# Kernel optimization log

Measured on AMD Instinct MI355X. Metric: run time of the kernel, lower is better.

The kernel has to match this reference:

```python
import jax, jax.numpy as jnp
import numpy as np

B, T, F = 16, 512, 512
H, D = 8, 64  # heads, key_dim (latent_dim)
EPS = 1e-3    # keras LayerNormalization default epsilon


def layer_norm(x, g, b):
    mu = jnp.mean(x, axis=-1, keepdims=True)
    var = jnp.mean(jnp.square(x - mu), axis=-1, keepdims=True)
    return (x - mu) * jax.lax.rsqrt(var + EPS) * g + b


def setup_inputs() -> dict:
    key = jax.random.key(0)
    ks = jax.random.split(key, 16)
    s = 0.02
    return {
        "x": jax.random.normal(ks[0], (B, T, F), jnp.float32),
        # MultiHeadAttention params (keras layout)
        "Wq": jax.random.normal(ks[1], (F, H, D), jnp.float32) * s,
        "bq": jnp.zeros((H, D), jnp.float32),
        "Wk": jax.random.normal(ks[2], (F, H, D), jnp.float32) * s,
        "bk": jnp.zeros((H, D), jnp.float32),
        "Wv": jax.random.normal(ks[3], (F, H, D), jnp.float32) * s,
        "bv": jnp.zeros((H, D), jnp.float32),
        "Wo": jax.random.normal(ks[4], (H, D, F), jnp.float32) * s,
        "bo": jnp.zeros((F,), jnp.float32),
        "ln1_g": jnp.ones((F,), jnp.float32),
        "ln1_b": jnp.zeros((F,), jnp.float32),
        # GRU (reset_after=True, recurrent_activation=sigmoid, activation=relu)
        "gru_k": jax.random.normal(ks[5], (F, 3 * F), jnp.float32) * s,
        "gru_rk": jax.random.normal(ks[6], (F, 3 * F), jnp.float32) * s,
        "gru_b": jnp.zeros((2, 3 * F), jnp.float32),  # [input_bias, recurrent_bias]
        # Dense
        "Wd": jax.random.normal(ks[7], (F, F), jnp.float32) * s,
        "bd": jnp.zeros((F,), jnp.float32),
        "ln2_g": jnp.ones((F,), jnp.float32),
        "ln2_b": jnp.zeros((F,), jnp.float32),
    }


def mha(x, Wq, bq, Wk, bk, Wv, bv, Wo, bo):
    q = jnp.einsum("btf,fhd->bthd", x, Wq) + bq
    k = jnp.einsum("bsf,fhd->bshd", x, Wk) + bk
    v = jnp.einsum("bsf,fhd->bshd", x, Wv) + bv
    scores = jnp.einsum("bthd,bshd->bhts", q, k) / jnp.sqrt(jnp.float32(D))
    attn = jax.nn.softmax(scores, axis=-1)
    ctx = jnp.einsum("bhts,bshd->bthd", attn, v)
    return jnp.einsum("bthd,hdf->btf", ctx, Wo) + bo


def gru(x, gru_k, gru_rk, gru_b):
    # keras GRU, reset_after=True: precompute input projections once
    xp = x @ gru_k + gru_b[0]            # [B,T,3F]
    rb = gru_b[1]                        # recurrent bias [3F]
    xp_t = jnp.transpose(xp, (1, 0, 2))  # time-major [T,B,3F]

    def step(h, xt):
        rec = h @ gru_rk + rb
        xz, xr, xh = jnp.split(xt, 3, axis=-1)
        rz, rr, rh = jnp.split(rec, 3, axis=-1)
        z = jax.nn.sigmoid(xz + rz)
        r = jax.nn.sigmoid(xr + rr)
        hh = jax.nn.relu(xh + r * rh)    # activation='relu'
        h_new = z * h + (1.0 - z) * hh
        return h_new, h_new

    h0 = jnp.zeros((x.shape[0], gru_rk.shape[0]), x.dtype)
    _, ys = jax.lax.scan(step, h0, xp_t)
    return jnp.transpose(ys, (1, 0, 2))  # [B,T,F]


def reference(x, Wq, bq, Wk, bk, Wv, bv, Wo, bo, ln1_g, ln1_b,
              gru_k, gru_rk, gru_b, Wd, bd, ln2_g, ln2_b):
    a = mha(x, Wq, bq, Wk, bk, Wv, bv, Wo, bo)
    x1 = layer_norm(a + x, ln1_g, ln1_b)
    g = gru(x1, gru_k, gru_rk, gru_b)
    d = g @ Wd + bd
    return layer_norm(d + x1, ln2_g, ln2_b)
```

## Files before the change

### kernel.cpp

```cpp
#include <hip/hip_runtime.h>
#include <math.h>

#define GRID_WGS 128

typedef __attribute__((ext_vector_type(8))) short bf16x8;
typedef __attribute__((ext_vector_type(4))) float f32x4;
typedef __attribute__((ext_vector_type(4))) unsigned short us4;

static __device__ __forceinline__ float sigmoidf_(float x) {
    return 1.0f / (1.0f + __expf(-x));
}
static __device__ __forceinline__ unsigned short f2bf(float f) {
    unsigned int u = __float_as_uint(f);
    u += 0x7fffu + ((u >> 16) & 1u);
    return (unsigned short)(u >> 16);
}
static __device__ __forceinline__ float bfbits2f(unsigned int b) {
    return __uint_as_float(b << 16);
}
static __device__ __forceinline__ void gload_lds16(const void* g, void* l) {
    __builtin_amdgcn_global_load_lds(
        (const __attribute__((address_space(1))) unsigned int*)g,
        (__attribute__((address_space(3))) unsigned int*)l, 16, 0, 0);
}

__global__ __launch_bounds__(256)
void prep(const float* __restrict__ x, unsigned short* __restrict__ xb,
          const float* __restrict__ bq, const float* __restrict__ bk,
          const float* __restrict__ bv, float* __restrict__ bqkv,
          const float* __restrict__ Wq, const float* __restrict__ Wk,
          const float* __restrict__ Wv, const float* __restrict__ Wo,
          const float* __restrict__ gruk, const float* __restrict__ Wd,
          unsigned short* __restrict__ wqkvT, unsigned short* __restrict__ woT,
          unsigned short* __restrict__ gkT, unsigned short* __restrict__ wdT,
          unsigned int* __restrict__ hbufz, unsigned int* __restrict__ Z)
{
    __shared__ float tile[32][33];
    const int bid = blockIdx.x, tid = threadIdx.x;
    if (bid < 4096) {
        const int i = (bid * 256 + tid) * 4;
        const float4 v = *(const float4*)(x + i);
        const us4 o = {f2bf(v.x), f2bf(v.y), f2bf(v.z), f2bf(v.w)};
        *(us4*)(xb + i) = o;
    } else if (bid < 4102) {
        const int i = (bid - 4096) * 256 + tid;
        bqkv[i] = (i < 512) ? bq[i] : ((i < 1024) ? bk[i - 512] : bv[i - 1024]);
    } else if (bid < 6150) {
        int t = bid - 4102;
        const float* in; unsigned short* out; int N;
        if      (t < 256)  { in = Wq;   out = wqkvT;               N = 512;  }
        else if (t < 512)  { in = Wk;   out = wqkvT + 256 * 1024;  N = 512;  t -= 256;  }
        else if (t < 768)  { in = Wv;   out = wqkvT + 512 * 1024;  N = 512;  t -= 512;  }
        else if (t < 1024) { in = Wo;   out = woT;                 N = 512;  t -= 768;  }
        else if (t < 1792) { in = gruk; out = gkT;                 N = 1536; t -= 1024; }
        else               { in = Wd;   out = wdT;                 N = 512;  t -= 1792; }
        const int tilesx = N / 32;
        const int n0 = (t % tilesx) * 32, k0 = (t / tilesx) * 32;
        const int c = tid & 31, r8 = tid >> 5;
#pragma unroll
        for (int i = 0; i < 4; ++i) {
            const int k = r8 + i * 8;
            tile[k][c] = in[(size_t)(k0 + k) * N + n0 + c];
        }
        __syncthreads();
#pragma unroll
        for (int i = 0; i < 4; ++i) {
            const int n = r8 + i * 8;
            out[(size_t)(n0 + n) * 512 + k0 + c] = f2bf(tile[c][n]);
        }
    } else if (bid == 6150) {
        for (int i = tid; i < 8192; i += 256) hbufz[i] = 0u;
    } else {
        for (int i = tid; i < 2048; i += 256) Z[i] = 0u;
    }
}

__global__ __launch_bounds__(256)
void gemm_bf16(const unsigned short* __restrict__ A, const unsigned short* __restrict__ Bt,
               const float* __restrict__ bias, const float* __restrict__ resid,
               float* __restrict__ C, unsigned short* __restrict__ Cb,
               int M, int N, int K)
{
    __shared__ unsigned short As[128 * 64];
    __shared__ unsigned short Bs[128 * 64];
    const int tid = threadIdx.x;
    const int wave = tid >> 6, lane = tid & 63;
    const int bm = blockIdx.x * 128, bn = blockIdx.y * 128;
    const int wr = wave >> 1, wc = wave & 1;
    const int stR = lane >> 3;
    const int stC = (lane & 7) * 8;

    const unsigned short* Abase = A + (size_t)(bm + wave * 32 + stR) * K + stC;
    const unsigned short* Bbase = Bt + (size_t)(bn + wave * 32 + stR) * K + stC;
    unsigned short* AsW = As + wave * 2048;
    unsigned short* BsW = Bs + wave * 2048;

    f32x4 acc[4][4] = {};
    const int fr = lane & 15;
    const int fko = (lane >> 4) * 8;

    for (int k0 = 0; k0 < K; k0 += 64) {
#pragma unroll
        for (int i = 0; i < 4; ++i) {
            gload_lds16(Abase + (size_t)i * 8 * K + k0, AsW + i * 512);
            gload_lds16(Bbase + (size_t)i * 8 * K + k0, BsW + i * 512);
        }
        __syncthreads();
        bf16x8 af[4][2], bfr[4][2];
#pragma unroll
        for (int m = 0; m < 4; ++m) {
            const unsigned short* ap = As + (wr * 64 + m * 16 + fr) * 64 + fko;
            af[m][0] = *(const bf16x8*)(ap);
            af[m][1] = *(const bf16x8*)(ap + 32);
        }
#pragma unroll
        for (int n = 0; n < 4; ++n) {
            const unsigned short* bp = Bs + (wc * 64 + n * 16 + fr) * 64 + fko;
            bfr[n][0] = *(const bf16x8*)(bp);
            bfr[n][1] = *(const bf16x8*)(bp + 32);
        }
#pragma unroll
        for (int m = 0; m < 4; ++m)
#pragma unroll
            for (int n = 0; n < 4; ++n) {
                acc[m][n] = __builtin_amdgcn_mfma_f32_16x16x32_bf16(af[m][0], bfr[n][0], acc[m][n], 0, 0, 0);
                acc[m][n] = __builtin_amdgcn_mfma_f32_16x16x32_bf16(af[m][1], bfr[n][1], acc[m][n], 0, 0, 0);
            }
        __syncthreads();
    }
    const int fq = lane >> 4;
#pragma unroll
    for (int n = 0; n < 4; ++n) {
        const int col = bn + wc * 64 + n * 16 + fr;
        const float bv = bias ? bias[col] : 0.f;
#pragma unroll
        for (int m = 0; m < 4; ++m) {
#pragma unroll
            for (int j = 0; j < 4; ++j) {
                const int row = bm + wr * 64 + m * 16 + fq * 4 + j;
                float v = acc[m][n][j] + bv;
                if (resid) v += resid[(size_t)row * N + col];
                if (C)  C[(size_t)row * N + col] = v;
                if (Cb) Cb[(size_t)row * N + col] = f2bf(v);
            }
        }
    }
}

__global__ __launch_bounds__(256)
void attn_bf16(const unsigned short* __restrict__ qkv, unsigned short* __restrict__ ctxb)
{
    __shared__ float S[64][512];
    __shared__ float KV[64][68];
    const int tid = threadIdx.x;
    const int wg = blockIdx.x;
    const int qt = wg & 7, h = (wg >> 3) & 7, b = wg >> 6;
    const int r = tid >> 2, quad = tid & 3;
    const int t0 = qt * 64;

    float4 qreg[16];
    {
        const unsigned short* qrow = qkv + ((size_t)(b * 512 + t0 + r) * 1536) + h * 64;
#pragma unroll
        for (int i = 0; i < 8; ++i) {
            const bf16x8 v = *(const bf16x8*)(qrow + i * 8);
            qreg[2 * i] = {bfbits2f((unsigned short)v[0]) * 0.125f,
                           bfbits2f((unsigned short)v[1]) * 0.125f,
                           bfbits2f((unsigned short)v[2]) * 0.125f,
                           bfbits2f((unsigned short)v[3]) * 0.125f};
            qreg[2 * i + 1] = {bfbits2f((unsigned short)v[4]) * 0.125f,
                               bfbits2f((unsigned short)v[5]) * 0.125f,
                               bfbits2f((unsigned short)v[6]) * 0.125f,
                               bfbits2f((unsigned short)v[7]) * 0.125f};
        }
    }
    for (int st = 0; st < 8; ++st) {
        {
            const int s = tid >> 2, d0 = quad * 16;
            const unsigned short* krow =
                qkv + ((size_t)(b * 512 + st * 64 + s) * 1536) + 512 + h * 64 + d0;
            const bf16x8 v0 = *(const bf16x8*)(krow);
            const bf16x8 v1 = *(const bf16x8*)(krow + 8);
#pragma unroll
            for (int e = 0; e < 8; ++e) {
                KV[s][d0 + e] = bfbits2f((unsigned short)v0[e]);
                KV[s][d0 + 8 + e] = bfbits2f((unsigned short)v1[e]);
            }
        }
        __syncthreads();
        const int sbase = quad * 16;
#pragma unroll 4
        for (int sp = 0; sp < 16; ++sp) {
            const int s = sbase + sp;
            float accd = 0.f;
#pragma unroll
            for (int kk = 0; kk < 16; ++kk) {
                const float4 kv = *(const float4*)&KV[s][kk * 4];
                accd += qreg[kk].x * kv.x + qreg[kk].y * kv.y +
                        qreg[kk].z * kv.z + qreg[kk].w * kv.w;
            }
            S[r][st * 64 + s] = accd;
        }
        __syncthreads();
    }
    const int c0 = quad * 128;
    float mx = -1e30f;
    for (int c4 = 0; c4 < 32; ++c4) {
        const float4 sv = *(const float4*)&S[r][c0 + c4 * 4];
        mx = fmaxf(mx, fmaxf(fmaxf(sv.x, sv.y), fmaxf(sv.z, sv.w)));
    }
    mx = fmaxf(mx, __shfl_xor(mx, 1));
    mx = fmaxf(mx, __shfl_xor(mx, 2));
    float sum = 0.f;
    for (int c4 = 0; c4 < 32; ++c4) {
        float4 sv = *(const float4*)&S[r][c0 + c4 * 4];
        sv.x = __expf(sv.x - mx); sv.y = __expf(sv.y - mx);
        sv.z = __expf(sv.z - mx); sv.w = __expf(sv.w - mx);
        sum += sv.x + sv.y + sv.z + sv.w;
        *(float4*)&S[r][c0 + c4 * 4] = sv;
    }
    sum += __shfl_xor(sum, 1);
    sum += __shfl_xor(sum, 2);
    const float inv = 1.0f / sum;
    __syncthreads();
    float o[16] = {};
    const int d0 = quad * 16;
    for (int st = 0; st < 8; ++st) {
        {
            const int s = tid >> 2;
            const unsigned short* vrow =
                qkv + ((size_t)(b * 512 + st * 64 + s) * 1536) + 1024 + h * 64 + d0;
            const bf16x8 v0 = *(const bf16x8*)(vrow);
            const bf16x8 v1 = *(const bf16x8*)(vrow + 8);
#pragma unroll
            for (int e = 0; e < 8; ++e) {
                KV[s][d0 + e] = bfbits2f((unsigned short)v0[e]);
                KV[s][d0 + 8 + e] = bfbits2f((unsigned short)v1[e]);
            }
        }
        __syncthreads();
        for (int s4 = 0; s4 < 16; ++s4) {
            const float4 p = *(const float4*)&S[r][st * 64 + s4 * 4];
            const float pv[4] = {p.x, p.y, p.z, p.w};
#pragma unroll
            for (int jj = 0; jj < 4; ++jj) {
                const int s = s4 * 4 + jj;
#pragma unroll
                for (int i = 0; i < 4; ++i) {
                    const float4 vv = *(const float4*)&KV[s][d0 + i * 4];
                    o[i * 4 + 0] = fmaf(pv[jj], vv.x, o[i * 4 + 0]);
                    o[i * 4 + 1] = fmaf(pv[jj], vv.y, o[i * 4 + 1]);
                    o[i * 4 + 2] = fmaf(pv[jj], vv.z, o[i * 4 + 2]);
                    o[i * 4 + 3] = fmaf(pv[jj], vv.w, o[i * 4 + 3]);
                }
            }
        }
        __syncthreads();
    }
    unsigned short* crow = ctxb + ((size_t)(b * 512 + t0 + r) * 512) + h * 64 + d0;
#pragma unroll
    for (int i = 0; i < 4; ++i) {
        const us4 t = {f2bf(o[i * 4 + 0] * inv), f2bf(o[i * 4 + 1] * inv),
                       f2bf(o[i * 4 + 2] * inv), f2bf(o[i * 4 + 3] * inv)};
        *(us4*)(crow + i * 4) = t;
    }
}

__global__ __launch_bounds__(256)
void ln_f32(const float* __restrict__ in, float* __restrict__ out,
            const float* __restrict__ g, const float* __restrict__ bb,
            unsigned short* __restrict__ outb)
{
    const int lane = threadIdx.x & 63;
    const int row = blockIdx.x * 4 + (threadIdx.x >> 6);
    const float* x = in + (size_t)row * 512;
    const float4 a = *(const float4*)(x + lane * 4);
    const float4 c = *(const float4*)(x + 256 + lane * 4);
    float s = a.x + a.y + a.z + a.w + c.x + c.y + c.z + c.w;
#pragma unroll
    for (int off = 1; off < 64; off <<= 1) s += __shfl_xor(s, off);
    const float mu = s * (1.0f / 512.0f);
    float vs = 0.f;
    vs += (a.x - mu) * (a.x - mu) + (a.y - mu) * (a.y - mu);
    vs += (a.z - mu) * (a.z - mu) + (a.w - mu) * (a.w - mu);
    vs += (c.x - mu) * (c.x - mu) + (c.y - mu) * (c.y - mu);
    vs += (c.z - mu) * (c.z - mu) + (c.w - mu) * (c.w - mu);
#pragma unroll
    for (int off = 1; off < 64; off <<= 1) vs += __shfl_xor(vs, off);
    const float rstd = rsqrtf(vs * (1.0f / 512.0f) + 1e-3f);
    const float4 g1 = *(const float4*)(g + lane * 4);
    const float4 g2 = *(const float4*)(g + 256 + lane * 4);
    const float4 b1 = *(const float4*)(bb + lane * 4);
    const float4 b2 = *(const float4*)(bb + 256 + lane * 4);
    float* y = out + (size_t)row * 512;
    const float4 o1 = {(a.x - mu) * rstd * g1.x + b1.x, (a.y - mu) * rstd * g1.y + b1.y,
                       (a.z - mu) * rstd * g1.z + b1.z, (a.w - mu) * rstd * g1.w + b1.w};
    const float4 o2 = {(c.x - mu) * rstd * g2.x + b2.x, (c.y - mu) * rstd * g2.y + b2.y,
                       (c.z - mu) * rstd * g2.z + b2.z, (c.w - mu) * rstd * g2.w + b2.w};
    *(float4*)(y + lane * 4) = o1;
    *(float4*)(y + 256 + lane * 4) = o2;
    if (outb) {
        unsigned short* yb = outb + (size_t)row * 512;
        const us4 p1 = {f2bf(o1.x), f2bf(o1.y), f2bf(o1.z), f2bf(o1.w)};
        const us4 p2 = {f2bf(o2.x), f2bf(o2.y), f2bf(o2.z), f2bf(o2.w)};
        *(us4*)(yb + lane * 4) = p1;
        *(us4*)(yb + 256 + lane * 4) = p2;
    }
}

__global__ __launch_bounds__(256, 1)
void gru_persist(const float* __restrict__ rk,
                 const unsigned short* __restrict__ xpb,
                 const float* __restrict__ rb,
                 unsigned short* __restrict__ hbuf,
                 unsigned short* __restrict__ goutb,
                 unsigned int* __restrict__ bar,
                 unsigned int* __restrict__ ctl)
{
    __shared__ int sh_part, sh_memb;
    const int tid = threadIdx.x;

    if (tid == 0) {
        unsigned int xcc;
        asm("s_getreg_b32 %0, hwreg(HW_REG_XCC_ID)" : "=s"(xcc));
        xcc &= 7u;
        const unsigned int rank =
            __hip_atomic_fetch_add(&ctl[xcc], 1u, __ATOMIC_RELAXED, __HIP_MEMORY_SCOPE_AGENT);
        __hip_atomic_fetch_add(&ctl[8], 1u, __ATOMIC_ACQ_REL, __HIP_MEMORY_SCOPE_AGENT);
        unsigned int spins = 0;
        while (__hip_atomic_load(&ctl[8], __ATOMIC_ACQUIRE, __HIP_MEMORY_SCOPE_AGENT)
               < (unsigned)GRID_WGS) {
            __builtin_amdgcn_s_sleep(1);
            if (++spins > (1u << 20)) break;
        }
        unsigned int cnt[8];
#pragma unroll
        for (int i = 0; i < 8; ++i)
            cnt[i] = __hip_atomic_load(&ctl[i], __ATOMIC_ACQUIRE, __HIP_MEMORY_SCOPE_AGENT);
        int best = 0;
#pragma unroll
        for (int i = 1; i < 8; ++i)
            if (cnt[i] > cnt[best]) best = i;
        sh_part = (xcc == (unsigned)best && rank < 8u) ? 1 : 0;
        sh_memb = (int)rank;
    }
    __syncthreads();
    if (!sh_part) return;
    const int member = sh_memb;

    const int wv = tid >> 6, l = tid & 63;
    const int wgi = member * 4 + wv;
    const int lo16 = l & 15;
    const int hi4 = l >> 4;
    const int gc = wgi * 16 + lo16;

    bf16x8 B[3][16];
#pragma unroll
    for (int g = 0; g < 3; ++g)
#pragma unroll
        for (int kt = 0; kt < 16; ++kt) {
            bf16x8 bv;
#pragma unroll
            for (int j = 0; j < 8; ++j) {
                const int k = kt * 32 + hi4 * 8 + j;
                bv[j] = (short)f2bf(rk[(size_t)k * 1536 + g * 512 + gc]);
            }
            B[g][kt] = bv;
        }
    const float rbz = rb[gc], rbr = rb[512 + gc], rbh = rb[1024 + gc];
    float hst[4] = {0.f, 0.f, 0.f, 0.f};

    unsigned int xnz[4], xnr[4], xnh[4];
#pragma unroll
    for (int j = 0; j < 4; ++j) {
        const unsigned short* xrow = xpb + ((size_t)((hi4 * 4 + j) * 512)) * 1536 + gc;
        xnz[j] = xrow[0]; xnr[j] = xrow[512]; xnh[j] = xrow[1024];
    }

    const unsigned short* ab0 = hbuf + lo16 * 512 + hi4 * 8;
    const unsigned short* ab1 = ab0 + 16 * 512;

    for (int t = 0; t < 512; ++t) {
        const unsigned short* abase = (t & 1) ? ab1 : ab0;
        unsigned short* hw = hbuf + (size_t)((t + 1) & 1) * (16 * 512);
        bf16x8 A[16];
        asm volatile(
            "global_load_dwordx4 %0,  %16, off sc0\n\t"
            "global_load_dwordx4 %1,  %16, off offset:64 sc0\n\t"
            "global_load_dwordx4 %2,  %16, off offset:128 sc0\n\t"
            "global_load_dwordx4 %3,  %16, off offset:192 sc0\n\t"
            "global_load_dwordx4 %4,  %16, off offset:256 sc0\n\t"
            "global_load_dwordx4 %5,  %16, off offset:320 sc0\n\t"
            "global_load_dwordx4 %6,  %16, off offset:384 sc0\n\t"
            "global_load_dwordx4 %7,  %16, off offset:448 sc0\n\t"
            "global_load_dwordx4 %8,  %16, off offset:512 sc0\n\t"
            "global_load_dwordx4 %9,  %16, off offset:576 sc0\n\t"
            "global_load_dwordx4 %10, %16, off offset:640 sc0\n\t"
            "global_load_dwordx4 %11, %16, off offset:704 sc0\n\t"
            "global_load_dwordx4 %12, %16, off offset:768 sc0\n\t"
            "global_load_dwordx4 %13, %16, off offset:832 sc0\n\t"
            "global_load_dwordx4 %14, %16, off offset:896 sc0\n\t"
            "global_load_dwordx4 %15, %16, off offset:960 sc0"
            : "=&v"(A[0]), "=&v"(A[1]), "=&v"(A[2]), "=&v"(A[3]),
              "=&v"(A[4]), "=&v"(A[5]), "=&v"(A[6]), "=&v"(A[7]),
              "=&v"(A[8]), "=&v"(A[9]), "=&v"(A[10]), "=&v"(A[11]),
              "=&v"(A[12]), "=&v"(A[13]), "=&v"(A[14]), "=&v"(A[15])
            : "v"(abase) : "memory");
        asm volatile("s_waitcnt vmcnt(0)" ::: "memory");
        __builtin_amdgcn_sched_barrier(0);
        float xz[4], xr[4], xh[4];
#pragma unroll
        for (int j = 0; j < 4; ++j) {
            xz[j] = bfbits2f(xnz[j]); xr[j] = bfbits2f(xnr[j]); xh[j] = bfbits2f(xnh[j]);
        }
        f32x4 accz = {0.f, 0.f, 0.f, 0.f};
        f32x4 accr = {0.f, 0.f, 0.f, 0.f};
        f32x4 acch = {0.f, 0.f, 0.f, 0.f};
#pragma unroll
        for (int kt = 0; kt < 16; ++kt) {
            accz = __builtin_amdgcn_mfma_f32_16x16x32_bf16(A[kt], B[0][kt], accz, 0, 0, 0);
            accr = __builtin_amdgcn_mfma_f32_16x16x32_bf16(A[kt], B[1][kt], accr, 0, 0, 0);
            acch = __builtin_amdgcn_mfma_f32_16x16x32_bf16(A[kt], B[2][kt], acch, 0, 0, 0);
        }
#pragma unroll
        for (int j = 0; j < 4; ++j) {
            const int b = hi4 * 4 + j;
            const float z = sigmoidf_(xz[j] + accz[j] + rbz);
            const float r = sigmoidf_(xr[j] + accr[j] + rbr);
            const float hh = fmaxf(xh[j] + r * (acch[j] + rbh), 0.f);
            const float hnew = z * hst[j] + (1.f - z) * hh;
            hst[j] = hnew;
            const unsigned short hb = f2bf(hnew);
            hw[b * 512 + gc] = hb;
            goutb[((size_t)(b * 512 + t)) * 512 + gc] = hb;
        }
        asm volatile("s_waitcnt vmcnt(0)" ::: "memory");
        __builtin_amdgcn_sched_barrier(0);
        if (t < 511) {
            {
                const unsigned short* x0 = xpb + ((size_t)((hi4 * 4 + 0) * 512 + t + 1)) * 1536 + gc;
                const unsigned short* x1 = xpb + ((size_t)((hi4 * 4 + 1) * 512 + t + 1)) * 1536 + gc;
                const unsigned short* x2 = xpb + ((size_t)((hi4 * 4 + 2) * 512 + t + 1)) * 1536 + gc;
                const unsigned short* x3 = xpb + ((size_t)((hi4 * 4 + 3) * 512 + t + 1)) * 1536 + gc;
                asm volatile(
                    "global_load_ushort %0,  %12, off\n\t"
                    "global_load_ushort %1,  %12, off offset:1024\n\t"
                    "global_load_ushort %2,  %12, off offset:2048\n\t"
                    "global_load_ushort %3,  %13, off\n\t"
                    "global_load_ushort %4,  %13, off offset:1024\n\t"
                    "global_load_ushort %5,  %13, off offset:2048\n\t"
                    "global_load_ushort %6,  %14, off\n\t"
                    "global_load_ushort %7,  %14, off offset:1024\n\t"
                    "global_load_ushort %8,  %14, off offset:2048\n\t"
                    "global_load_ushort %9,  %15, off\n\t"
                    "global_load_ushort %10, %15, off offset:1024\n\t"
                    "global_load_ushort %11, %15, off offset:2048"
                    : "=&v"(xnz[0]), "=&v"(xnr[0]), "=&v"(xnh[0]),
                      "=&v"(xnz[1]), "=&v"(xnr[1]), "=&v"(xnh[1]),
                      "=&v"(xnz[2]), "=&v"(xnr[2]), "=&v"(xnh[2]),
                      "=&v"(xnz[3]), "=&v"(xnr[3]), "=&v"(xnh[3])
                    : "v"(x0), "v"(x1), "v"(x2), "v"(x3) : "memory");
            }
            __syncthreads();
            if (tid == 0) {
                __hip_atomic_fetch_add(bar, 1u, __ATOMIC_RELAXED, __HIP_MEMORY_SCOPE_AGENT);
                const unsigned int target = 8u * (unsigned int)(t + 1);
                unsigned int it = 0;
                while (__hip_atomic_load(bar, __ATOMIC_RELAXED, __HIP_MEMORY_SCOPE_AGENT)
                       < target) {
                    if (++it > (1u << 14)) break;
                }
                if (it > (1u << 14)) {
                    unsigned int cur = 0, it2 = 0;
                    do {
                        asm volatile("global_atomic_add %0, %1, %2, off sc0\n\t"
                                     "s_waitcnt vmcnt(0)"
                                     : "=v"(cur) : "v"(bar), "v"(0u) : "memory");
                        if (++it2 > (1u << 15)) break;
                    } while (cur < target);
                }
            }
            __syncthreads();
        }
    }
}

extern "C" void kernel_launch(void* const* d_in, const int* in_sizes, int n_in,
                              void* d_out, int out_size, void* d_ws, size_t ws_size,
                              hipStream_t stream)
{
    const float* x     = (const float*)d_in[0];
    const float* Wq    = (const float*)d_in[1];
    const float* bq    = (const float*)d_in[2];
    const float* Wk    = (const float*)d_in[3];
    const float* bk    = (const float*)d_in[4];
    const float* Wv    = (const float*)d_in[5];
    const float* bv    = (const float*)d_in[6];
    const float* Wo    = (const float*)d_in[7];
    const float* bo    = (const float*)d_in[8];
    const float* ln1g  = (const float*)d_in[9];
    const float* ln1b  = (const float*)d_in[10];
    const float* gruk  = (const float*)d_in[11];
    const float* grurk = (const float*)d_in[12];
    const float* grub  = (const float*)d_in[13];
    const float* Wd    = (const float*)d_in[14];
    const float* bd    = (const float*)d_in[15];
    const float* ln2g  = (const float*)d_in[16];
    const float* ln2b  = (const float*)d_in[17];
    float* out = (float*)d_out;

    char* base = (char*)d_ws;
    const size_t MB = 1024 * 1024;
    unsigned short* qkvb = (unsigned short*)base;
    unsigned short* xpb  = (unsigned short*)base;
    float*          dout = (float*)(base + 24 * MB);
    float*          R4   = (float*)(base + 48 * MB);
    unsigned short* S1   = (unsigned short*)(base + 64 * MB);
    unsigned short* WT   = (unsigned short*)(base + 72 * MB);
    unsigned short* wqkvT = WT;
    unsigned short* woT  = WT + 768 * 1024;
    unsigned short* gkT  = WT + 1024 * 1024;
    unsigned short* wdT  = WT + 1792 * 1024;
    unsigned short* hbuf = (unsigned short*)(base + 76 * MB);
    char*           Z    = base + 76 * MB + 64 * 1024;
    unsigned int*   ctl  = (unsigned int*)(Z);
    unsigned int*   bar  = (unsigned int*)(Z + 256);
    float*          bqkv = (float*)(base + 77 * MB);

    const dim3 blk(256);
    const dim3 g512(8192 / 128, 512 / 128);
    const dim3 g1536(8192 / 128, 1536 / 128);

    prep<<<dim3(6152), blk, 0, stream>>>(x, S1, bq, bk, bv, bqkv,
                                         Wq, Wk, Wv, Wo, gruk, Wd,
                                         wqkvT, woT, gkT, wdT,
                                         (unsigned int*)hbuf, (unsigned int*)Z);
    gemm_bf16<<<g1536, blk, 0, stream>>>(S1, wqkvT, bqkv, nullptr, nullptr, qkvb, 8192, 1536, 512);
    attn_bf16<<<dim3(1024), blk, 0, stream>>>(qkvb, S1);
    gemm_bf16<<<g512, blk, 0, stream>>>(S1, woT, bo, x, R4, nullptr, 8192, 512, 512);
    ln_f32<<<dim3(2048), blk, 0, stream>>>(R4, R4, ln1g, ln1b, S1);
    gemm_bf16<<<g1536, blk, 0, stream>>>(S1, gkT, grub, nullptr, nullptr, xpb, 8192, 1536, 512);
    gru_persist<<<dim3(GRID_WGS), blk, 0, stream>>>(grurk, xpb, grub + 1536, hbuf, S1, bar, ctl);
    gemm_bf16<<<g512, blk, 0, stream>>>(S1, wdT, bd, R4, dout, nullptr, 8192, 512, 512);
    ln_f32<<<dim3(2048), blk, 0, stream>>>(dout, out, ln2g, ln2b, nullptr);
}
```

Baseline: 2.333 ms.

## Shrink attention tiles with bf16 score storage; defer GRU output stores and prefetch

The attention kernel now handles 32 query rows per workgroup instead of 64, launching twice as many blocks. It keeps the score matrix in bf16 to cut shared memory, and each thread covers 8 keys or 8 output dims with reuse of K/V loads. In the GRU recurrence, the next step's input loads and the previous step's output stores are issued together with the hidden-state loads, so their latency overlaps the matvec; the final step's store moves after the loop. Storing probabilities in bf16 lowers softmax precision, and the partial vmcnt wait relies on exact instruction counts.

```diff
diff --git a/kernel.cpp b/kernel.cpp
--- a/kernel.cpp
+++ b/kernel.cpp
@@ -150,13 +150,14 @@
 __global__ __launch_bounds__(256)
 void attn_bf16(const unsigned short* __restrict__ qkv, unsigned short* __restrict__ ctxb)
 {
-    __shared__ float S[64][512];
-    __shared__ float KV[64][68];
+    __shared__ unsigned short S[32][512];
+    __shared__ float KV[64][69];
     const int tid = threadIdx.x;
     const int wg = blockIdx.x;
-    const int qt = wg & 7, h = (wg >> 3) & 7, b = wg >> 6;
-    const int r = tid >> 2, quad = tid & 3;
-    const int t0 = qt * 64;
+    const int qt = wg & 15, h = (wg >> 4) & 7, b = wg >> 7;
+    const int r = tid >> 3, oct = tid & 7;
+    const int t0 = qt * 32;
+    const int ss = tid >> 2, d4 = (tid & 3) * 16;
 
     float4 qreg[16];
     {
@@ -176,94 +177,97 @@
     }
     for (int st = 0; st < 8; ++st) {
         {
-            const int s = tid >> 2, d0 = quad * 16;
             const unsigned short* krow =
-                qkv + ((size_t)(b * 512 + st * 64 + s) * 1536) + 512 + h * 64 + d0;
+                qkv + ((size_t)(b * 512 + st * 64 + ss) * 1536) + 512 + h * 64 + d4;
             const bf16x8 v0 = *(const bf16x8*)(krow);
             const bf16x8 v1 = *(const bf16x8*)(krow + 8);
 #pragma unroll
             for (int e = 0; e < 8; ++e) {
-                KV[s][d0 + e] = bfbits2f((unsigned short)v0[e]);
-                KV[s][d0 + 8 + e] = bfbits2f((unsigned short)v1[e]);
-            }
-        }
-        __syncthreads();
-        const int sbase = quad * 16;
+                KV[ss][d4 + e] = bfbits2f((unsigned short)v0[e]);
+                KV[ss][d4 + 8 + e] = bfbits2f((unsigned short)v1[e]);
+            }
+        }
+        __syncthreads();
+        float accd[8] = {};
 #pragma unroll 4
-        for (int sp = 0; sp < 16; ++sp) {
-            const int s = sbase + sp;
-            float accd = 0.f;
-#pragma unroll
-            for (int kk = 0; kk < 16; ++kk) {
-                const float4 kv = *(const float4*)&KV[s][kk * 4];
-                accd += qreg[kk].x * kv.x + qreg[kk].y * kv.y +
-                        qreg[kk].z * kv.z + qreg[kk].w * kv.w;
-            }
-            S[r][st * 64 + s] = accd;
-        }
-        __syncthreads();
-    }
-    const int c0 = quad * 128;
+        for (int kk = 0; kk < 16; ++kk) {
+            const float4 qv = qreg[kk];
+#pragma unroll
+            for (int i = 0; i < 8; ++i) {
+                const float4 kv = *(const float4*)&KV[oct * 8 + i][kk * 4];
+                accd[i] += qv.x * kv.x + qv.y * kv.y + qv.z * kv.z + qv.w * kv.w;
+            }
+        }
+#pragma unroll
+        for (int i = 0; i < 8; ++i)
+            S[r][st * 64 + oct * 8 + i] = f2bf(accd[i]);
+        __syncthreads();
+    }
+    const int c0 = oct * 64;
     float mx = -1e30f;
-    for (int c4 = 0; c4 < 32; ++c4) {
-        const float4 sv = *(const float4*)&S[r][c0 + c4 * 4];
-        mx = fmaxf(mx, fmaxf(fmaxf(sv.x, sv.y), fmaxf(sv.z, sv.w)));
+#pragma unroll
+    for (int c8 = 0; c8 < 8; ++c8) {
+        const bf16x8 sv = *(const bf16x8*)&S[r][c0 + c8 * 8];
+#pragma unroll
+        for (int e = 0; e < 8; ++e) mx = fmaxf(mx, bfbits2f((unsigned short)sv[e]));
     }
     mx = fmaxf(mx, __shfl_xor(mx, 1));
     mx = fmaxf(mx, __shfl_xor(mx, 2));
+    mx = fmaxf(mx, __shfl_xor(mx, 4));
     float sum = 0.f;
-    for (int c4 = 0; c4 < 32; ++c4) {
-        float4 sv = *(const float4*)&S[r][c0 + c4 * 4];
-        sv.x = __expf(sv.x - mx); sv.y = __expf(sv.y - mx);
-        sv.z = __expf(sv.z - mx); sv.w = __expf(sv.w - mx);
-        sum += sv.x + sv.y + sv.z + sv.w;
-        *(float4*)&S[r][c0 + c4 * 4] = sv;
+#pragma unroll
+    for (int c8 = 0; c8 < 8; ++c8) {
+        const bf16x8 sv = *(const bf16x8*)&S[r][c0 + c8 * 8];
+        us4 o1, o2;
+#pragma unroll
+        for (int e = 0; e < 8; ++e) {
+            const float p = __expf(bfbits2f((unsigned short)sv[e]) - mx);
+            sum += p;
+            if (e < 4) o1[e] = f2bf(p); else o2[e - 4] = f2bf(p);
+        }
+        *(us4*)&S[r][c0 + c8 * 8] = o1;
+        *(us4*)&S[r][c0 + c8 * 8 + 4] = o2;
     }
     sum += __shfl_xor(sum, 1);
     sum += __shfl_xor(sum, 2);
+    sum += __shfl_xor(sum, 4);
     const float inv = 1.0f / sum;
     __syncthreads();
-    float o[16] = {};
-    const int d0 = quad * 16;
+    float o[8] = {};
     for (int st = 0; st < 8; ++st) {
         {
-            const int s = tid >> 2;
             const unsigned short* vrow =
-                qkv + ((size_t)(b * 512 + st * 64 + s) * 1536) + 1024 + h * 64 + d0;
+                qkv + ((size_t)(b * 512 + st * 64 + ss) * 1536) + 1024 + h * 64 + d4;
             const bf16x8 v0 = *(const bf16x8*)(vrow);
             const bf16x8 v1 = *(const bf16x8*)(vrow + 8);
 #pragma unroll
             for (int e = 0; e < 8; ++e) {
-                KV[s][d0 + e] = bfbits2f((unsigned short)v0[e]);
-                KV[s][d0 + 8 + e] = bfbits2f((unsigned short)v1[e]);
-            }
-        }
-        __syncthreads();
-        for (int s4 = 0; s4 < 16; ++s4) {
-            const float4 p = *(const float4*)&S[r][st * 64 + s4 * 4];
-            const float pv[4] = {p.x, p.y, p.z, p.w};
-#pragma unroll
-            for (int jj = 0; jj < 4; ++jj) {
-                const int s = s4 * 4 + jj;
-#pragma unroll
-                for (int i = 0; i < 4; ++i) {
-                    const float4 vv = *(const float4*)&KV[s][d0 + i * 4];
-                    o[i * 4 + 0] = fmaf(pv[jj], vv.x, o[i * 4 + 0]);
-                    o[i * 4 + 1] = fmaf(pv[jj], vv.y, o[i * 4 + 1]);
-                    o[i * 4 + 2] = fmaf(pv[jj], vv.z, o[i * 4 + 2]);
-                    o[i * 4 + 3] = fmaf(pv[jj], vv.w, o[i * 4 + 3]);
-                }
-            }
-        }
-        __syncthreads();
-    }
-    unsigned short* crow = ctxb + ((size_t)(b * 512 + t0 + r) * 512) + h * 64 + d0;
-#pragma unroll
-    for (int i = 0; i < 4; ++i) {
-        const us4 t = {f2bf(o[i * 4 + 0] * inv), f2bf(o[i * 4 + 1] * inv),
-                       f2bf(o[i * 4 + 2] * inv), f2bf(o[i * 4 + 3] * inv)};
-        *(us4*)(crow + i * 4) = t;
-    }
+                KV[ss][d4 + e] = bfbits2f((unsigned short)v0[e]);
+                KV[ss][d4 + 8 + e] = bfbits2f((unsigned short)v1[e]);
+            }
+        }
+        __syncthreads();
+#pragma unroll 2
+        for (int s8 = 0; s8 < 8; ++s8) {
+            const bf16x8 pv = *(const bf16x8*)&S[r][st * 64 + s8 * 8];
+#pragma unroll
+            for (int e = 0; e < 8; ++e) {
+                const float p = bfbits2f((unsigned short)pv[e]);
+                const float4 k0 = *(const float4*)&KV[s8 * 8 + e][oct * 8];
+                const float4 k1 = *(const float4*)&KV[s8 * 8 + e][oct * 8 + 4];
+                o[0] = fmaf(p, k0.x, o[0]); o[1] = fmaf(p, k0.y, o[1]);
+                o[2] = fmaf(p, k0.z, o[2]); o[3] = fmaf(p, k0.w, o[3]);
+                o[4] = fmaf(p, k1.x, o[4]); o[5] = fmaf(p, k1.y, o[5]);
+                o[6] = fmaf(p, k1.z, o[6]); o[7] = fmaf(p, k1.w, o[7]);
+            }
+        }
+        __syncthreads();
+    }
+    unsigned short* crow = ctxb + ((size_t)(b * 512 + t0 + r) * 512) + h * 64 + oct * 8;
+    const us4 t1 = {f2bf(o[0] * inv), f2bf(o[1] * inv), f2bf(o[2] * inv), f2bf(o[3] * inv)};
+    const us4 t2 = {f2bf(o[4] * inv), f2bf(o[5] * inv), f2bf(o[6] * inv), f2bf(o[7] * inv)};
+    *(us4*)(crow) = t1;
+    *(us4*)(crow + 4) = t2;
 }
 
 __global__ __launch_bounds__(256)
@@ -370,12 +374,13 @@
     const float rbz = rb[gc], rbr = rb[512 + gc], rbh = rb[1024 + gc];
     float hst[4] = {0.f, 0.f, 0.f, 0.f};
 
-    unsigned int xnz[4], xnr[4], xnh[4];
+    float xz[4], xr[4], xh[4];
 #pragma unroll
     for (int j = 0; j < 4; ++j) {
         const unsigned short* xrow = xpb + ((size_t)((hi4 * 4 + j) * 512)) * 1536 + gc;
-        xnz[j] = xrow[0]; xnr[j] = xrow[512]; xnh[j] = xrow[1024];
-    }
+        xz[j] = bfbits2f(xrow[0]); xr[j] = bfbits2f(xrow[512]); xh[j] = bfbits2f(xrow[1024]);
+    }
+    unsigned int hnb[4] = {0u, 0u, 0u, 0u};
 
     const unsigned short* ab0 = hbuf + lo16 * 512 + hi4 * 8;
     const unsigned short* ab1 = ab0 + 16 * 512;
@@ -406,13 +411,48 @@
               "=&v"(A[8]), "=&v"(A[9]), "=&v"(A[10]), "=&v"(A[11]),
               "=&v"(A[12]), "=&v"(A[13]), "=&v"(A[14]), "=&v"(A[15])
             : "v"(abase) : "memory");
-        asm volatile("s_waitcnt vmcnt(0)" ::: "memory");
+        unsigned int xnz[4], xnr[4], xnh[4];
+        {
+            const unsigned short* x0 = xpb + ((size_t)((hi4 * 4 + 0) * 512 + t + 1)) * 1536 + gc;
+            const unsigned short* x1 = xpb + ((size_t)((hi4 * 4 + 1) * 512 + t + 1)) * 1536 + gc;
+            const unsigned short* x2 = xpb + ((size_t)((hi4 * 4 + 2) * 512 + t + 1)) * 1536 + gc;
+            const unsigned short* x3 = xpb + ((size_t)((hi4 * 4 + 3) * 512 + t + 1)) * 1536 + gc;
+            asm volatile(
+                "global_load_ushort %0,  %12, off\n\t"
+                "global_load_ushort %1,  %12, off offset:1024\n\t"
+                "global_load_ushort %2,  %12, off offset:2048\n\t"
+                "global_load_ushort %3,  %13, off\n\t"
+                "global_load_ushort %4,  %13, off offset:1024\n\t"
+                "global_load_ushort %5,  %13, off offset:2048\n\t"
+                "global_load_ushort %6,  %14, off\n\t"
+                "global_load_ushort %7,  %14, off offset:1024\n\t"
+                "global_load_ushort %8,  %14, off offset:2048\n\t"
+                "global_load_ushort %9,  %15, off\n\t"
+                "global_load_ushort %10, %15, off offset:1024\n\t"
+                "global_load_ushort %11, %15, off offset:2048"
+                : "=&v"(xnz[0]), "=&v"(xnr[0]), "=&v"(xnh[0]),
+                  "=&v"(xnz[1]), "=&v"(xnr[1]), "=&v"(xnh[1]),
+                  "=&v"(xnz[2]), "=&v"(xnr[2]), "=&v"(xnh[2]),
+                  "=&v"(xnz[3]), "=&v"(xnr[3]), "=&v"(xnh[3])
+                : "v"(x0), "v"(x1), "v"(x2), "v"(x3) : "memory");
+        }
+        {
+            const int grow = t ? t - 1 : 0;
+            unsigned short* g0 = goutb + ((size_t)((hi4 * 4 + 0) * 512 + grow)) * 512 + gc;
+            unsigned short* g1 = goutb + ((size_t)((hi4 * 4 + 1) * 512 + grow)) * 512 + gc;
+            unsigned short* g2 = goutb + ((size_t)((hi4 * 4 + 2) * 512 + grow)) * 512 + gc;
+            unsigned short* g3 = goutb + ((size_t)((hi4 * 4 + 3) * 512 + grow)) * 512 + gc;
+            asm volatile(
+                "global_store_short %0, %4, off\n\t"
+                "global_store_short %1, %5, off\n\t"
+                "global_store_short %2, %6, off\n\t"
+                "global_store_short %3, %7, off"
+                :: "v"(g0), "v"(g1), "v"(g2), "v"(g3),
+                   "v"(hnb[0]), "v"(hnb[1]), "v"(hnb[2]), "v"(hnb[3]) : "memory");
+        }
+        asm volatile("s_waitcnt vmcnt(16)" ::: "memory");
         __builtin_amdgcn_sched_barrier(0);
-        float xz[4], xr[4], xh[4];
-#pragma unroll
-        for (int j = 0; j < 4; ++j) {
-            xz[j] = bfbits2f(xnz[j]); xr[j] = bfbits2f(xnr[j]); xh[j] = bfbits2f(xnh[j]);
-        }
+
         f32x4 accz = {0.f, 0.f, 0.f, 0.f};
         f32x4 accr = {0.f, 0.f, 0.f, 0.f};
         f32x4 acch = {0.f, 0.f, 0.f, 0.f};
@@ -431,36 +471,16 @@
             const float hnew = z * hst[j] + (1.f - z) * hh;
             hst[j] = hnew;
             const unsigned short hb = f2bf(hnew);
+            hnb[j] = (unsigned int)hb;
             hw[b * 512 + gc] = hb;
-            goutb[((size_t)(b * 512 + t)) * 512 + gc] = hb;
         }
         asm volatile("s_waitcnt vmcnt(0)" ::: "memory");
         __builtin_amdgcn_sched_barrier(0);
+#pragma unroll
+        for (int j = 0; j < 4; ++j) {
+            xz[j] = bfbits2f(xnz[j]); xr[j] = bfbits2f(xnr[j]); xh[j] = bfbits2f(xnh[j]);
+        }
         if (t < 511) {
-            {
-                const unsigned short* x0 = xpb + ((size_t)((hi4 * 4 + 0) * 512 + t + 1)) * 1536 + gc;
-                const unsigned short* x1 = xpb + ((size_t)((hi4 * 4 + 1) * 512 + t + 1)) * 1536 + gc;
-                const unsigned short* x2 = xpb + ((size_t)((hi4 * 4 + 2) * 512 + t + 1)) * 1536 + gc;
-                const unsigned short* x3 = xpb + ((size_t)((hi4 * 4 + 3) * 512 + t + 1)) * 1536 + gc;
-                asm volatile(
-                    "global_load_ushort %0,  %12, off\n\t"
-                    "global_load_ushort %1,  %12, off offset:1024\n\t"
-                    "global_load_ushort %2,  %12, off offset:2048\n\t"
-                    "global_load_ushort %3,  %13, off\n\t"
-                    "global_load_ushort %4,  %13, off offset:1024\n\t"
-                    "global_load_ushort %5,  %13, off offset:2048\n\t"
-                    "global_load_ushort %6,  %14, off\n\t"
-                    "global_load_ushort %7,  %14, off offset:1024\n\t"
-                    "global_load_ushort %8,  %14, off offset:2048\n\t"
-                    "global_load_ushort %9,  %15, off\n\t"
-                    "global_load_ushort %10, %15, off offset:1024\n\t"
-                    "global_load_ushort %11, %15, off offset:2048"
-                    : "=&v"(xnz[0]), "=&v"(xnr[0]), "=&v"(xnh[0]),
-                      "=&v"(xnz[1]), "=&v"(xnr[1]), "=&v"(xnh[1]),
-                      "=&v"(xnz[2]), "=&v"(xnr[2]), "=&v"(xnh[2]),
-                      "=&v"(xnz[3]), "=&v"(xnr[3]), "=&v"(xnh[3])
-                    : "v"(x0), "v"(x1), "v"(x2), "v"(x3) : "memory");
-            }
             __syncthreads();
             if (tid == 0) {
                 __hip_atomic_fetch_add(bar, 1u, __ATOMIC_RELAXED, __HIP_MEMORY_SCOPE_AGENT);
@@ -483,6 +503,9 @@
             __syncthreads();
         }
     }
+#pragma unroll
+    for (int j = 0; j < 4; ++j)
+        goutb[((size_t)((hi4 * 4 + j) * 512 + 511)) * 512 + gc] = (unsigned short)hnb[j];
 }
 
 extern "C" void kernel_launch(void* const* d_in, const int* in_sizes, int n_in,
@@ -536,7 +559,7 @@
                                          wqkvT, woT, gkT, wdT,
                                          (unsigned int*)hbuf, (unsigned int*)Z);
     gemm_bf16<<<g1536, blk, 0, stream>>>(S1, wqkvT, bqkv, nullptr, nullptr, qkvb, 8192, 1536, 512);
-    attn_bf16<<<dim3(1024), blk, 0, stream>>>(qkvb, S1);
+    attn_bf16<<<dim3(2048), blk, 0, stream>>>(qkvb, S1);
     gemm_bf16<<<g512, blk, 0, stream>>>(S1, woT, bo, x, R4, nullptr, 8192, 512, 512);
     ln_f32<<<dim3(2048), blk, 0, stream>>>(R4, R4, ln1g, ln1b, S1);
     gemm_bf16<<<g1536, blk, 0, stream>>>(S1, gkT, grub, nullptr, nullptr, xpb, 8192, 1536, 512);
```

After: 2.317 ms. Within noise of the previous version (-0.7%).
